# Optimization experiments

Hardware: AMD Instinct MI355X
Metric: run time of the kernel (lower is better)

The kernel has to match this reference:

```python
import jax, jax.numpy as jnp
import numpy as np


def _conv1x1(x, w, b):
    # x: (B,C,H,W), w: (O,C), b: (O,)
    return jnp.einsum('oc,bchw->bohw', w, x) + b[None, :, None, None]


def _avg_pool2(x):
    B, C, H, W = x.shape
    return x.reshape(B, C, H // 2, 2, W // 2, 2).mean(axis=(3, 5))


def setup_inputs() -> dict:
    key = jax.random.key(0)
    B, C, H, W = 8, 64, 64, 64
    ks = jax.random.split(key, 14)
    s = 1.0 / np.sqrt(C)

    def wb(k1, k2):
        return (jax.random.uniform(k1, (C, C), jnp.float32, -s, s),
                jax.random.uniform(k2, (C,), jnp.float32, -s, s))

    w_q, b_q = wb(ks[0], ks[1])
    w_K, b_K = wb(ks[2], ks[3])
    w_V, b_V = wb(ks[4], ks[5])
    w_Q, b_Q = wb(ks[6], ks[7])
    w_k, b_k = wb(ks[8], ks[9])
    w_v, b_v = wb(ks[10], ks[11])
    x = jax.random.normal(ks[12], (B, C, H, W), jnp.float32)
    gamma = jnp.ones((1,), jnp.float32)
    return dict(x=x, w_q=w_q, b_q=b_q, w_K=w_K, b_K=b_K, w_V=w_V, b_V=b_V,
                w_Q=w_Q, b_Q=b_Q, w_k=w_k, b_k=b_k, w_v=w_v, b_v=b_v,
                gamma=gamma)


def reference(x, w_q, b_q, w_K, b_K, w_V, b_V, w_Q, b_Q, w_k, b_k, w_v, b_v, gamma):
    B, C, H, W = x.shape
    N = H * W
    N4 = N // 4

    # Stage 1: pooled queries vs full key/value
    q = _conv1x1(x, w_q, b_q)                      # (B,C,H,W); torch views as (B,C,W,H) but H==W
    qp = _avg_pool2(q).reshape(B, C, N4).transpose(0, 2, 1)   # (B,N/4,C)
    Kf = _conv1x1(x, w_K, b_K).reshape(B, C, N)                # (B,C,N)
    Vf = _conv1x1(x, w_V, b_V).reshape(B, C, N)                # (B,C,N)
    attn = jax.nn.softmax(jnp.einsum('bnc,bcm->bnm', qp, Kf), axis=-1)  # (B,N/4,N)
    out = jnp.einsum('bcm,bnm->bcn', Vf, attn)                 # (B,C,N/4)
    out = out.reshape(B, C, H // 2, W // 2)

    # Stage 2: full queries vs pooled-derived key/value
    Qf = _conv1x1(x, w_Q, b_Q).reshape(B, C, N).transpose(0, 2, 1)  # (B,N,C)
    kp = _conv1x1(out, w_k, b_k).reshape(B, C, N4)                  # (B,C,N/4)
    vp = _conv1x1(out, w_v, b_v).reshape(B, C, N4)                  # (B,C,N/4)
    attn2 = jax.nn.softmax(jnp.einsum('bnc,bcm->bnm', Qf, kp), axis=-1)  # (B,N,N/4)
    out2 = jnp.einsum('bcm,bnm->bcn', vp, attn2).reshape(B, C, H, W)

    return gamma * out2 + x
```

## Files before the change

kernel.cpp:

```cpp
#include <hip/hip_runtime.h>
#include <math.h>


typedef __bf16 bf16;
typedef __attribute__((ext_vector_type(4))) __bf16 bf16x4;
typedef __attribute__((ext_vector_type(8))) __bf16 bf16x8;
typedef __attribute__((ext_vector_type(4))) float f32x4;

__device__ __forceinline__ void gl_lds16(const bf16* g, bf16* l) {
    __builtin_amdgcn_global_load_lds(
        (const __attribute__((address_space(1))) unsigned int*)g,
        (__attribute__((address_space(3))) unsigned int*)l,
        16, 0, 0);
}

__device__ __forceinline__ void proj_wave(
    const bf16* __restrict__ src, int TN,
    const float* __restrict__ W, const float* __restrict__ Bs,
    bf16* __restrict__ Y, int tr, int N, int b, int gn0, int lane)
{
    const int c16 = lane & 15, q4 = lane >> 4;
    bf16x8 wa[4][2];
    #pragma unroll
    for (int to = 0; to < 4; ++to)
        #pragma unroll
        for (int h = 0; h < 2; ++h) {
            const float* wp = W + (16 * to + c16) * 64 + q4 * 8 + 32 * h;
            float4 f0 = *(const float4*)wp;
            float4 f1 = *(const float4*)(wp + 4);
            bf16 tmp[8] = {(bf16)f0.x, (bf16)f0.y, (bf16)f0.z, (bf16)f0.w,
                           (bf16)f1.x, (bf16)f1.y, (bf16)f1.z, (bf16)f1.w};
            wa[to][h] = *(bf16x8*)tmp;
        }
    for (int tn = 0; tn < TN; ++tn) {
        bf16x8 xb0 = *(const bf16x8*)&src[(16 * tn + c16) * 72 + q4 * 8];
        bf16x8 xb1 = *(const bf16x8*)&src[(16 * tn + c16) * 72 + q4 * 8 + 32];
        #pragma unroll
        for (int to = 0; to < 4; ++to) {
            f32x4 acc = (f32x4){0.f, 0.f, 0.f, 0.f};
            acc = __builtin_amdgcn_mfma_f32_16x16x32_bf16(wa[to][0], xb0, acc, 0, 0, 0);
            acc = __builtin_amdgcn_mfma_f32_16x16x32_bf16(wa[to][1], xb1, acc, 0, 0, 0);
            if (tr) {
                float4 b4 = *(const float4*)(Bs + 16 * to + q4 * 4);
                bf16x4 yv;
                yv[0] = (bf16)(acc[0] + b4.x); yv[1] = (bf16)(acc[1] + b4.y);
                yv[2] = (bf16)(acc[2] + b4.z); yv[3] = (bf16)(acc[3] + b4.w);
                *(bf16x4*)(Y + ((size_t)b * N + gn0 + 16 * tn + c16) * 64 + 16 * to + q4 * 4) = yv;
            } else {
                float4 b4 = *(const float4*)(Bs + 16 * to + q4 * 4);
                float bias[4] = {b4.x, b4.y, b4.z, b4.w};
                #pragma unroll
                for (int r = 0; r < 4; ++r)
                    Y[((size_t)b * 64 + 16 * to + q4 * 4 + r) * N + gn0 + 16 * tn + c16] =
                        (bf16)(acc[r] + bias[r]);
            }
        }
    }
}

__global__ __launch_bounds__(256) void prep_kernel(
    const float* __restrict__ x,
    const float* __restrict__ w_K, const float* __restrict__ b_K, bf16* __restrict__ Kt,
    const float* __restrict__ w_Q, const float* __restrict__ b_Q, bf16* __restrict__ Qt,
    const float* __restrict__ w_V, const float* __restrict__ b_V, bf16* __restrict__ Vf,
    const float* __restrict__ w_q, const float* __restrict__ b_q, bf16* __restrict__ qpt)
{
    __shared__ float tile[128 * 65];
    __shared__ __align__(16) bf16 xbT[128 * 72];
    __shared__ __align__(16) bf16 xpb[32 * 72];
    const int t  = threadIdx.x;
    const int h2 = blockIdx.x;
    const int b  = blockIdx.y;
    const int n0 = h2 * 128;

    #pragma unroll
    for (int i = 0; i < 32; ++i) {
        int lin = i * 256 + t;
        int n = lin & 127, c = lin >> 7;
        tile[n * 65 + c] = x[((size_t)b * 64 + c) * 4096 + n0 + n];
    }
    __syncthreads();
    #pragma unroll
    for (int i = 0; i < 4; ++i) {
        int slot = i * 256 + t;
        int n = slot >> 3, c0 = (slot & 7) * 8;
        bf16 tmp[8];
        #pragma unroll
        for (int j = 0; j < 8; ++j) tmp[j] = (bf16)tile[n * 65 + c0 + j];
        *(bf16x8*)&xbT[n * 72 + c0] = *(bf16x8*)tmp;
    }
    {
        int wp = t & 31, c0 = (t >> 5) * 8;
        bf16 tmp[8];
        #pragma unroll
        for (int j = 0; j < 8; ++j) {
            float a = tile[(2 * wp) * 65 + c0 + j] + tile[(2 * wp + 1) * 65 + c0 + j]
                    + tile[(64 + 2 * wp) * 65 + c0 + j] + tile[(64 + 2 * wp + 1) * 65 + c0 + j];
            tmp[j] = (bf16)(0.25f * a);
        }
        *(bf16x8*)&xpb[wp * 72 + c0] = *(bf16x8*)tmp;
    }
    __syncthreads();

    const int lane = t & 63;
    const int w    = t >> 6;
    {
        const int mat  = w >> 1;
        const int half = w & 1;
        proj_wave(xbT + half * 64 * 72, 4,
                  mat == 0 ? w_K : w_Q, mat == 0 ? b_K : b_Q,
                  mat == 0 ? Kt : Qt, 1, 4096, b, n0 + half * 64, lane);
    }
    if (w < 2) {
        proj_wave(xbT + w * 64 * 72, 4, w_V, b_V, Vf, 0, 4096, b, n0 + w * 64, lane);
    } else if (w == 2) {
        proj_wave(xpb, 2, w_q, b_q, qpt, 1, 1024, b, h2 * 32, lane);
    }
}

template<int NSPLIT, int PLAYOUT>
__global__ __launch_bounds__(256, 3) void flash_kernel(
    const bf16* __restrict__ Qt, const bf16* __restrict__ Kt,
    const bf16* __restrict__ Vn, int NQ, int L,
    bf16* __restrict__ Opart, float* __restrict__ Mbuf, float* __restrict__ Lbuf)
{
    const int tid  = threadIdx.x;
    const int lane = tid & 63;
    const int w    = tid >> 6;
    const int c16  = lane & 15;
    const int q4   = lane >> 4;
    const int b    = blockIdx.y;
    const int n0   = blockIdx.x * 128 + w * 32;
    const int s    = blockIdx.z;
    const int SL   = L / NSPLIT;
    const int k0   = s * SL;
    const int ntiles = SL / 64;

    __shared__ __align__(16) bf16 Ks[2][64 * 64];
    __shared__ __align__(16) bf16 Vs[2][64 * 64];
    __shared__ __align__(16) bf16 Pw[4][32 * 72];

    const int rl8 = lane >> 3;
    const int cg  = ((lane & 7) - rl8) & 7;

    const bf16* Kb = Kt + (size_t)b * L * 64;
    const bf16* Vb = Vn + (size_t)b * 64 * L;

    bf16x8 bq[2][2];
    #pragma unroll
    for (int u = 0; u < 2; ++u) {
        const bf16* qrow = Qt + ((size_t)b * NQ + n0 + 16 * u + c16) * 64 + q4 * 8;
        bq[u][0] = *(const bf16x8*)(qrow);
        bq[u][1] = *(const bf16x8*)(qrow + 32);
    }

    f32x4 O[2][4];
    #pragma unroll
    for (int u = 0; u < 2; ++u)
        #pragma unroll
        for (int g = 0; g < 4; ++g) O[u][g] = (f32x4){0.f, 0.f, 0.f, 0.f};
    float m_run[2] = {-INFINITY, -INFINITY};
    float l_run[2] = {0.f, 0.f};

    #pragma unroll
    for (int j = 0; j < 2; ++j) {
        const int row = 16 * w + 8 * j + rl8;
        gl_lds16(Kb + (size_t)(k0 + row) * 64 + cg * 8, &Ks[0][(16 * w + 8 * j) * 64]);
        gl_lds16(Vb + (size_t)row * L + k0 + cg * 8,    &Vs[0][(16 * w + 8 * j) * 64]);
    }
    __syncthreads();

    for (int it = 0; it < ntiles; ++it) {
        const int buf = it & 1;
        if (it + 1 < ntiles) {
            const int kn = k0 + (it + 1) * 64;
            #pragma unroll
            for (int j = 0; j < 2; ++j) {
                const int row = 16 * w + 8 * j + rl8;
                gl_lds16(Kb + (size_t)(kn + row) * 64 + cg * 8, &Ks[buf ^ 1][(16 * w + 8 * j) * 64]);
                gl_lds16(Vb + (size_t)row * L + kn + cg * 8,    &Vs[buf ^ 1][(16 * w + 8 * j) * 64]);
            }
        }

        f32x4 sv[2][4];
        #pragma unroll
        for (int t = 0; t < 4; ++t) {
            const bf16* krow = &Ks[buf][(16 * t + c16) * 64];
            bf16x8 ak0 = *(const bf16x8*)&krow[((q4 + c16) & 7) * 8];
            bf16x8 ak1 = *(const bf16x8*)&krow[((q4 + 4 + c16) & 7) * 8];
            #pragma unroll
            for (int u = 0; u < 2; ++u) {
                f32x4 z = (f32x4){0.f, 0.f, 0.f, 0.f};
                z = __builtin_amdgcn_mfma_f32_16x16x32_bf16(ak0, bq[u][0], z, 0, 0, 0);
                sv[u][t] = __builtin_amdgcn_mfma_f32_16x16x32_bf16(ak1, bq[u][1], z, 0, 0, 0);
            }
        }

        #pragma unroll
        for (int u = 0; u < 2; ++u) {
            float mx = sv[u][0][0];
            #pragma unroll
            for (int t = 0; t < 4; ++t)
                #pragma unroll
                for (int r = 0; r < 4; ++r) mx = fmaxf(mx, sv[u][t][r]);
            mx = fmaxf(mx, __shfl_xor(mx, 16));
            mx = fmaxf(mx, __shfl_xor(mx, 32));
            float nm = fmaxf(m_run[u], mx);
            float alpha = __expf(m_run[u] - nm);
            m_run[u] = nm;

            float ls = 0.f;
            #pragma unroll
            for (int t = 0; t < 4; ++t)
                #pragma unroll
                for (int r = 0; r < 4; ++r) {
                    float p = __expf(sv[u][t][r] - nm);
                    sv[u][t][r] = p;
                    ls += p;
                }
            ls += __shfl_xor(ls, 16);
            ls += __shfl_xor(ls, 32);
            l_run[u] = l_run[u] * alpha + ls;
            #pragma unroll
            for (int g = 0; g < 4; ++g)
                #pragma unroll
                for (int r = 0; r < 4; ++r) O[u][g][r] *= alpha;

            #pragma unroll
            for (int t = 0; t < 4; ++t) {
                bf16x4 pv;
                pv[0] = (bf16)sv[u][t][0]; pv[1] = (bf16)sv[u][t][1];
                pv[2] = (bf16)sv[u][t][2]; pv[3] = (bf16)sv[u][t][3];
                *(bf16x4*)&Pw[w][(16 * u + c16) * 72 + 16 * t + 4 * q4] = pv;
            }
        }

        #pragma unroll
        for (int h = 0; h < 2; ++h) {
            bf16x8 pf0 = *(const bf16x8*)&Pw[w][(c16) * 72 + 32 * h + 8 * q4];
            bf16x8 pf1 = *(const bf16x8*)&Pw[w][(16 + c16) * 72 + 32 * h + 8 * q4];
            #pragma unroll
            for (int g = 0; g < 4; ++g) {
                bf16x8 av = *(const bf16x8*)&Vs[buf][(16 * g + c16) * 64 + ((4 * h + q4 + c16) & 7) * 8];
                O[0][g] = __builtin_amdgcn_mfma_f32_16x16x32_bf16(av, pf0, O[0][g], 0, 0, 0);
                O[1][g] = __builtin_amdgcn_mfma_f32_16x16x32_bf16(av, pf1, O[1][g], 0, 0, 0);
            }
        }
        __syncthreads();
    }

    #pragma unroll
    for (int u = 0; u < 2; ++u) {
        float inv = 1.0f / l_run[u];
        if (PLAYOUT == 1) {
            bf16* dst = Opart + ((size_t)(b * NSPLIT + s) * NQ + n0 + 16 * u + c16) * 64 + q4 * 4;
            #pragma unroll
            for (int g = 0; g < 4; ++g) {
                bf16x4 yv;
                #pragma unroll
                for (int r = 0; r < 4; ++r) yv[r] = (bf16)(O[u][g][r] * inv);
                *(bf16x4*)(dst + 16 * g) = yv;
            }
        } else {
            #pragma unroll
            for (int g = 0; g < 4; ++g)
                #pragma unroll
                for (int r = 0; r < 4; ++r)
                    Opart[((size_t)(b * NSPLIT + s) * 64 + 16 * g + 4 * q4 + r) * NQ + n0 + 16 * u + c16] =
                        (bf16)(O[u][g][r] * inv);
        }
    }
    if (lane < 16) {
        #pragma unroll
        for (int u = 0; u < 2; ++u) {
            Mbuf[(b * NSPLIT + s) * NQ + n0 + 16 * u + lane] = m_run[u];
            Lbuf[(b * NSPLIT + s) * NQ + n0 + 16 * u + lane] = l_run[u];
        }
    }
}

__global__ __launch_bounds__(256) void comb1kv_kernel(
    const bf16* __restrict__ Opart, const float* __restrict__ Mbuf,
    const float* __restrict__ Lbuf,
    const float* __restrict__ w_k, const float* __restrict__ b_k, bf16* __restrict__ kpt,
    const float* __restrict__ w_v, const float* __restrict__ b_v, bf16* __restrict__ vp)
{
    __shared__ __align__(16) bf16 tile[32 * 72];
    __shared__ float wbuf[32 * 8];
    const int t  = threadIdx.x;
    const int m0 = blockIdx.x * 32;
    const int b  = blockIdx.y;

    if (t < 32) {
        int m = m0 + t;
        float ms[8], ls[8];
        #pragma unroll
        for (int s = 0; s < 8; ++s) {
            ms[s] = Mbuf[(b * 8 + s) * 1024 + m];
            ls[s] = Lbuf[(b * 8 + s) * 1024 + m];
        }
        float M = ms[0];
        #pragma unroll
        for (int s = 1; s < 8; ++s) M = fmaxf(M, ms[s]);
        float wsv[8], lt = 0.f;
        #pragma unroll
        for (int s = 0; s < 8; ++s) { wsv[s] = ls[s] * __expf(ms[s] - M); lt += wsv[s]; }
        float inv = 1.f / lt;
        #pragma unroll
        for (int s = 0; s < 8; ++s) wbuf[t * 8 + s] = wsv[s] * inv;
    }
    __syncthreads();

    #pragma unroll
    for (int i = 0; i < 2; ++i) {
        int ml = i * 16 + (t >> 4);
        int c4 = (t & 15) * 4;
        const bf16* base = Opart + ((size_t)(b * 8) * 1024 + m0 + ml) * 64 + c4;
        float a0 = 0.f, a1 = 0.f, a2 = 0.f, a3 = 0.f;
        #pragma unroll
        for (int s = 0; s < 8; ++s) {
            bf16x4 v = *(const bf16x4*)(base + (size_t)s * 1024 * 64);
            float wg = wbuf[ml * 8 + s];
            a0 += (float)v[0] * wg; a1 += (float)v[1] * wg;
            a2 += (float)v[2] * wg; a3 += (float)v[3] * wg;
        }
        bf16x4 o; o[0] = (bf16)a0; o[1] = (bf16)a1; o[2] = (bf16)a2; o[3] = (bf16)a3;
        *(bf16x4*)&tile[ml * 72 + c4] = o;
    }
    __syncthreads();

    const int lane = t & 63;
    const int w    = t >> 6;
    const int c16 = lane & 15, q4 = lane >> 4;

    if (w < 2) {
        bf16x8 wb[4][2];
        #pragma unroll
        for (int to = 0; to < 4; ++to)
            #pragma unroll
            for (int h = 0; h < 2; ++h) {
                const float* wp = w_k + (16 * to + c16) * 64 + q4 * 8 + 32 * h;
                float4 f0 = *(const float4*)wp;
                float4 f1 = *(const float4*)(wp + 4);
                bf16 tmp[8] = {(bf16)f0.x, (bf16)f0.y, (bf16)f0.z, (bf16)f0.w,
                               (bf16)f1.x, (bf16)f1.y, (bf16)f1.z, (bf16)f1.w};
                wb[to][h] = *(bf16x8*)tmp;
            }
        const int tm = w;
        bf16x8 a0 = *(const bf16x8*)&tile[(16 * tm + c16) * 72 + q4 * 8];
        bf16x8 a1 = *(const bf16x8*)&tile[(16 * tm + c16) * 72 + q4 * 8 + 32];
        #pragma unroll
        for (int to = 0; to < 4; ++to) {
            f32x4 acc = (f32x4){0.f, 0.f, 0.f, 0.f};
            acc = __builtin_amdgcn_mfma_f32_16x16x32_bf16(a0, wb[to][0], acc, 0, 0, 0);
            acc = __builtin_amdgcn_mfma_f32_16x16x32_bf16(a1, wb[to][1], acc, 0, 0, 0);
            float bias = b_k[16 * to + c16];
            #pragma unroll
            for (int r = 0; r < 4; ++r)
                kpt[((size_t)b * 1024 + m0 + 16 * tm + 4 * q4 + r) * 64 + 16 * to + c16] =
                    (bf16)(acc[r] + bias);
        }
    } else {
        bf16x8 wa[4][2];
        #pragma unroll
        for (int ta = 0; ta < 4; ++ta)
            #pragma unroll
            for (int h = 0; h < 2; ++h) {
                const float* wp = w_v + (16 * ta + c16) * 64 + q4 * 8 + 32 * h;
                float4 f0 = *(const float4*)wp;
                float4 f1 = *(const float4*)(wp + 4);
                bf16 tmp[8] = {(bf16)f0.x, (bf16)f0.y, (bf16)f0.z, (bf16)f0.w,
                               (bf16)f1.x, (bf16)f1.y, (bf16)f1.z, (bf16)f1.w};
                wa[ta][h] = *(bf16x8*)tmp;
            }
        const int tm = w - 2;
        bf16x8 bb0 = *(const bf16x8*)&tile[(16 * tm + c16) * 72 + q4 * 8];
        bf16x8 bb1 = *(const bf16x8*)&tile[(16 * tm + c16) * 72 + q4 * 8 + 32];
        #pragma unroll
        for (int ta = 0; ta < 4; ++ta) {
            f32x4 acc = (f32x4){0.f, 0.f, 0.f, 0.f};
            acc = __builtin_amdgcn_mfma_f32_16x16x32_bf16(wa[ta][0], bb0, acc, 0, 0, 0);
            acc = __builtin_amdgcn_mfma_f32_16x16x32_bf16(wa[ta][1], bb1, acc, 0, 0, 0);
            float4 b4 = *(const float4*)(b_v + 16 * ta + 4 * q4);
            float bias[4] = {b4.x, b4.y, b4.z, b4.w};
            #pragma unroll
            for (int r = 0; r < 4; ++r)
                vp[((size_t)b * 64 + 16 * ta + 4 * q4 + r) * 1024 + m0 + 16 * tm + c16] =
                    (bf16)(acc[r] + bias[r]);
        }
    }
}

__global__ __launch_bounds__(256) void combine2_kernel(
    const bf16* __restrict__ Opart, const float* __restrict__ Mbuf,
    const float* __restrict__ Lbuf, const float* __restrict__ x,
    const float* __restrict__ gamma_p, float* __restrict__ out)
{
    int idx = blockIdx.x * 256 + threadIdx.x;
    int n = idx & 4095;
    int b = idx >> 18;
    int c = (idx >> 12) & 63;
    float m0 = Mbuf[(b * 2 + 0) * 4096 + n], m1 = Mbuf[(b * 2 + 1) * 4096 + n];
    float l0 = Lbuf[(b * 2 + 0) * 4096 + n], l1 = Lbuf[(b * 2 + 1) * 4096 + n];
    float M = fmaxf(m0, m1);
    float w0 = l0 * __expf(m0 - M), w1 = l1 * __expf(m1 - M);
    float acc = (float)Opart[((size_t)(b * 2 + 0) * 64 + c) * 4096 + n] * w0
              + (float)Opart[((size_t)(b * 2 + 1) * 64 + c) * 4096 + n] * w1;
    out[idx] = gamma_p[0] * (acc / (w0 + w1)) + x[idx];
}

extern "C" void kernel_launch(void* const* d_in, const int* in_sizes, int n_in,
                              void* d_out, int out_size, void* d_ws, size_t ws_size,
                              hipStream_t stream) {
    const float* x    = (const float*)d_in[0];
    const float* w_q  = (const float*)d_in[1];
    const float* b_q  = (const float*)d_in[2];
    const float* w_K  = (const float*)d_in[3];
    const float* b_K  = (const float*)d_in[4];
    const float* w_V  = (const float*)d_in[5];
    const float* b_V  = (const float*)d_in[6];
    const float* w_Q  = (const float*)d_in[7];
    const float* b_Q  = (const float*)d_in[8];
    const float* w_k  = (const float*)d_in[9];
    const float* b_k  = (const float*)d_in[10];
    const float* w_v  = (const float*)d_in[11];
    const float* b_v  = (const float*)d_in[12];
    const float* gamma = (const float*)d_in[13];
    float* out = (float*)d_out;

    char* ws = (char*)d_ws;
    bf16*  Kt    = (bf16*)ws;   ws += (size_t)8 * 4096 * 64 * 2;
    bf16*  Qt    = (bf16*)ws;   ws += (size_t)8 * 4096 * 64 * 2;
    bf16*  Vf    = (bf16*)ws;   ws += (size_t)8 * 4096 * 64 * 2;
    bf16*  qpt   = (bf16*)ws;   ws += (size_t)8 * 1024 * 64 * 2;
    bf16*  kpt   = (bf16*)ws;   ws += (size_t)8 * 1024 * 64 * 2;
    bf16*  vp    = (bf16*)ws;   ws += (size_t)8 * 64 * 1024 * 2;
    bf16*  Opart = (bf16*)ws;   ws += (size_t)8 * 8 * 1024 * 64 * 2;
    float* Mb    = (float*)ws;  ws += (size_t)8 * 8 * 1024 * 4;
    float* Lb    = (float*)ws;  ws += (size_t)8 * 8 * 1024 * 4;

    prep_kernel<<<dim3(32, 8), 256, 0, stream>>>(
        x, w_K, b_K, Kt, w_Q, b_Q, Qt, w_V, b_V, Vf, w_q, b_q, qpt);

    flash_kernel<8, 1><<<dim3(8, 8, 8), 256, 0, stream>>>(
        qpt, Kt, Vf, 1024, 4096, Opart, Mb, Lb);

    comb1kv_kernel<<<dim3(32, 8), 256, 0, stream>>>(
        Opart, Mb, Lb, w_k, b_k, kpt, w_v, b_v, vp);

    flash_kernel<2, 0><<<dim3(32, 8, 2), 256, 0, stream>>>(
        Qt, kpt, vp, 4096, 1024, Opart, Mb, Lb);

    combine2_kernel<<<8192, 256, 0, stream>>>(Opart, Mb, Lb, x, gamma, out);
}
```

Before: 149.3 us.

## Drop split-K in stage-2 flash attention and fuse residual epilogue

The second attention pass now runs unsplit (NSPLIT=1) and writes the final fp32 output directly, applying gamma and adding the residual x in the flash kernel epilogue. This removes the separate combine2 kernel launch and the bf16 partial-output, max and sum round-trip through global memory. In exchange the grid for stage 2 halves (256 blocks), so each block walks the full 1024-key length and there is less parallelism. Output precision also improves slightly because the bf16 partial rounding is gone.

```diff
diff --git a/kernel.cpp b/kernel.cpp
--- a/kernel.cpp
+++ b/kernel.cpp
@@ -118,11 +118,13 @@
     }
 }
 
-template<int NSPLIT, int PLAYOUT>
+template<int NSPLIT, int MODE>
 __global__ __launch_bounds__(256, 3) void flash_kernel(
     const bf16* __restrict__ Qt, const bf16* __restrict__ Kt,
     const bf16* __restrict__ Vn, int NQ, int L,
-    bf16* __restrict__ Opart, float* __restrict__ Mbuf, float* __restrict__ Lbuf)
+    bf16* __restrict__ Opart, float* __restrict__ Mbuf, float* __restrict__ Lbuf,
+    float* __restrict__ out_f, const float* __restrict__ resid,
+    const float* __restrict__ gamma_p)
 {
     const int tid  = threadIdx.x;
     const int lane = tid & 63;
@@ -131,7 +133,7 @@
     const int q4   = lane >> 4;
     const int b    = blockIdx.y;
     const int n0   = blockIdx.x * 128 + w * 32;
-    const int s    = blockIdx.z;
+    const int s    = (NSPLIT > 1) ? blockIdx.z : 0;
     const int SL   = L / NSPLIT;
     const int k0   = s * SL;
     const int ntiles = SL / 64;
@@ -249,10 +251,25 @@
         __syncthreads();
     }
 
-    #pragma unroll
-    for (int u = 0; u < 2; ++u) {
-        float inv = 1.0f / l_run[u];
-        if (PLAYOUT == 1) {
+    if (MODE == 2) {
+        const float gm = gamma_p[0];
+        #pragma unroll
+        for (int u = 0; u < 2; ++u) {
+            float inv = gm / l_run[u];
+            const int n = n0 + 16 * u + c16;
+            #pragma unroll
+            for (int g = 0; g < 4; ++g) {
+                #pragma unroll
+                for (int r = 0; r < 4; ++r) {
+                    size_t oidx = ((size_t)b * 64 + 16 * g + 4 * q4 + r) * NQ + n;
+                    out_f[oidx] = O[u][g][r] * inv + resid[oidx];
+                }
+            }
+        }
+    } else {
+        #pragma unroll
+        for (int u = 0; u < 2; ++u) {
+            float inv = 1.0f / l_run[u];
             bf16* dst = Opart + ((size_t)(b * NSPLIT + s) * NQ + n0 + 16 * u + c16) * 64 + q4 * 4;
             #pragma unroll
             for (int g = 0; g < 4; ++g) {
@@ -261,20 +278,13 @@
                 for (int r = 0; r < 4; ++r) yv[r] = (bf16)(O[u][g][r] * inv);
                 *(bf16x4*)(dst + 16 * g) = yv;
             }
-        } else {
-            #pragma unroll
-            for (int g = 0; g < 4; ++g)
-                #pragma unroll
-                for (int r = 0; r < 4; ++r)
-                    Opart[((size_t)(b * NSPLIT + s) * 64 + 16 * g + 4 * q4 + r) * NQ + n0 + 16 * u + c16] =
-                        (bf16)(O[u][g][r] * inv);
-        }
-    }
-    if (lane < 16) {
-        #pragma unroll
-        for (int u = 0; u < 2; ++u) {
-            Mbuf[(b * NSPLIT + s) * NQ + n0 + 16 * u + lane] = m_run[u];
-            Lbuf[(b * NSPLIT + s) * NQ + n0 + 16 * u + lane] = l_run[u];
+        }
+        if (lane < 16) {
+            #pragma unroll
+            for (int u = 0; u < 2; ++u) {
+                Mbuf[(b * NSPLIT + s) * NQ + n0 + 16 * u + lane] = m_run[u];
+                Lbuf[(b * NSPLIT + s) * NQ + n0 + 16 * u + lane] = l_run[u];
+            }
         }
     }
 }
@@ -389,24 +399,6 @@
                     (bf16)(acc[r] + bias[r]);
         }
     }
-}
-
-__global__ __launch_bounds__(256) void combine2_kernel(
-    const bf16* __restrict__ Opart, const float* __restrict__ Mbuf,
-    const float* __restrict__ Lbuf, const float* __restrict__ x,
-    const float* __restrict__ gamma_p, float* __restrict__ out)
-{
-    int idx = blockIdx.x * 256 + threadIdx.x;
-    int n = idx & 4095;
-    int b = idx >> 18;
-    int c = (idx >> 12) & 63;
-    float m0 = Mbuf[(b * 2 + 0) * 4096 + n], m1 = Mbuf[(b * 2 + 1) * 4096 + n];
-    float l0 = Lbuf[(b * 2 + 0) * 4096 + n], l1 = Lbuf[(b * 2 + 1) * 4096 + n];
-    float M = fmaxf(m0, m1);
-    float w0 = l0 * __expf(m0 - M), w1 = l1 * __expf(m1 - M);
-    float acc = (float)Opart[((size_t)(b * 2 + 0) * 64 + c) * 4096 + n] * w0
-              + (float)Opart[((size_t)(b * 2 + 1) * 64 + c) * 4096 + n] * w1;
-    out[idx] = gamma_p[0] * (acc / (w0 + w1)) + x[idx];
 }
 
 extern "C" void kernel_launch(void* const* d_in, const int* in_sizes, int n_in,
@@ -443,13 +435,11 @@
         x, w_K, b_K, Kt, w_Q, b_Q, Qt, w_V, b_V, Vf, w_q, b_q, qpt);
 
     flash_kernel<8, 1><<<dim3(8, 8, 8), 256, 0, stream>>>(
-        qpt, Kt, Vf, 1024, 4096, Opart, Mb, Lb);
+        qpt, Kt, Vf, 1024, 4096, Opart, Mb, Lb, nullptr, nullptr, nullptr);
 
     comb1kv_kernel<<<dim3(32, 8), 256, 0, stream>>>(
         Opart, Mb, Lb, w_k, b_k, kpt, w_v, b_v, vp);
 
-    flash_kernel<2, 0><<<dim3(32, 8, 2), 256, 0, stream>>>(
-        Qt, kpt, vp, 4096, 1024, Opart, Mb, Lb);
-
-    combine2_kernel<<<8192, 256, 0, stream>>>(Opart, Mb, Lb, x, gamma, out);
-}
+    flash_kernel<1, 2><<<dim3(32, 8, 1), 256, 0, stream>>>(
+        Qt, kpt, vp, 4096, 1024, nullptr, nullptr, nullptr, out, x, gamma);
+}
```

After: 148.0 us. About the same (-0.8%).
